# Performance work log

Measured on AMD Instinct MI355X. Metric: run time of the kernel, lower is better.

Reference implementation:

```python
import jax, jax.numpy as jnp
import numpy as np

B, S, HID = 2, 2048, 2048
NH, NKV, HD = 8, 1, 256
G = NH // NKV  # key-value groups
ROPE_BASE = 10000.0


def _rope_tables(seq_len, dim, base=ROPE_BASE):
    inv_freq = 1.0 / (base ** (jnp.arange(0, dim, 2, dtype=jnp.float32) / dim))
    t = jnp.arange(seq_len, dtype=jnp.float32)
    freqs = jnp.outer(t, inv_freq)            # [S, dim/2]
    emb = jnp.concatenate([freqs, freqs], -1)  # [S, dim]
    return jnp.cos(emb), jnp.sin(emb)


def _rotate_half(x):
    x1, x2 = jnp.split(x, 2, axis=-1)
    return jnp.concatenate([-x2, x1], axis=-1)


def setup_inputs() -> dict:
    key = jax.random.key(0)
    ks = jax.random.split(key, 6)
    hidden_states = jax.random.normal(ks[0], (B, S, HID), dtype=jnp.float32)
    # additive causal mask (0 on/below diagonal, -1e9 above)
    causal = jnp.triu(jnp.full((S, S), -1e9, dtype=jnp.float32), k=1)
    attention_mask = jnp.broadcast_to(causal[None, None], (B, 1, S, S))
    sc = 0.02
    Wq = jax.random.normal(ks[1], (HID, NH * HD), dtype=jnp.float32) * sc
    Wk = jax.random.normal(ks[2], (HID, NKV * HD), dtype=jnp.float32) * sc
    Wv = jax.random.normal(ks[3], (HID, NKV * HD), dtype=jnp.float32) * sc
    Wo = jax.random.normal(ks[4], (NH * HD, HID), dtype=jnp.float32) * sc
    return {"hidden_states": hidden_states, "attention_mask": attention_mask,
            "Wq": Wq, "Wk": Wk, "Wv": Wv, "Wo": Wo}


def reference(hidden_states, attention_mask, Wq, Wk, Wv, Wo):
    b, s, _ = hidden_states.shape
    q = (hidden_states @ Wq).reshape(b, s, NH, HD).transpose(0, 2, 1, 3)    # [B,NH,S,D]
    k = (hidden_states @ Wk).reshape(b, s, NKV, HD).transpose(0, 2, 1, 3)   # [B,NKV,S,D]
    v = (hidden_states @ Wv).reshape(b, s, NKV, HD).transpose(0, 2, 1, 3)
    cos, sin = _rope_tables(s, HD)
    cos, sin = cos[None, None], sin[None, None]
    q = q * cos + _rotate_half(q) * sin
    k = k * cos + _rotate_half(k) * sin
    # GQA: broadcast KV over groups instead of repeat_interleave (same math)
    qg = q.reshape(b, NKV, G, s, HD)
    scores = jnp.einsum('bkgqd,bkld->bkgql', qg, k) / np.sqrt(HD)  # [B,NKV,G,S,S]
    scores = scores + attention_mask[:, :, None]                    # mask broadcast over kv/groups
    probs = jax.nn.softmax(scores, axis=-1)
    out = jnp.einsum('bkgql,bkld->bkgqd', probs, v)                 # [B,NKV,G,S,D]
    out = out.reshape(b, NH, s, HD).transpose(0, 2, 1, 3).reshape(b, s, NH * HD)
    return out @ Wo
```

## Files before the change

kernel.cpp:

```cpp
#include <hip/hip_runtime.h>
#include <hip/hip_bf16.h>
#include <cstdint>
#include <cstddef>

#define DEVI __device__ __forceinline__

typedef __attribute__((ext_vector_type(8))) short short8;
typedef __attribute__((ext_vector_type(4))) float f32x4;

constexpr int BB = 2, SS = 2048, HID = 2048, NH = 8, HD = 256;
constexpr int M_TOT = BB * SS;
constexpr int RTOT = BB * NH * SS;

DEVI unsigned short f2bf(float f) {
  union { float f; unsigned int u; } v; v.f = f;
  unsigned int u = v.u;
  unsigned int r = (u + 0x7FFFu + ((u >> 16) & 1u)) >> 16;
  return (unsigned short)r;
}

DEVI float bf2f(unsigned short u) {
  union { unsigned int i; float f; } v; v.i = ((unsigned int)u) << 16;
  return v.f;
}

DEVI void gload_lds16(const void* g, void* l) {
  __builtin_amdgcn_global_load_lds(
      (const __attribute__((address_space(1))) unsigned int*)g,
      (__attribute__((address_space(3))) unsigned int*)l, 16, 0, 0);
}

__global__ void convert_f32_bf16(const float* __restrict__ in,
                                 unsigned short* __restrict__ out, int n8) {
  const int i = blockIdx.x * blockDim.x + threadIdx.x;
  if (i >= n8) return;
  const f32x4* p = (const f32x4*)in;
  f32x4 a = p[i * 2], b = p[i * 2 + 1];
  short8 o;
#pragma unroll
  for (int j = 0; j < 4; ++j) {
    o[j] = (short)f2bf(a[j]);
    o[j + 4] = (short)f2bf(b[j]);
  }
  ((short8*)out)[i] = o;
}

__global__ void transpose_w(const float* __restrict__ W,
                            unsigned short* __restrict__ Wt, int K, int N) {
  __shared__ float t[32][33];
  const int n0 = blockIdx.x * 32, k0 = blockIdx.y * 32;
  const int c = threadIdx.x & 31, r8 = threadIdx.x >> 5;
#pragma unroll
  for (int i = 0; i < 4; ++i) {
    const int r = r8 + i * 8;
    t[r][c] = W[(size_t)(k0 + r) * N + n0 + c];
  }
  __syncthreads();
#pragma unroll
  for (int i = 0; i < 4; ++i) {
    const int r = r8 + i * 8;
    Wt[(size_t)(n0 + r) * K + k0 + c] = f2bf(t[c][r]);
  }
}

__global__ void rope_table(float* __restrict__ ct, float* __restrict__ st) {
  const int i = blockIdx.x * blockDim.x + threadIdx.x;
  const int s = i >> 7, d = i & 127;
  const float inv = __expf(-(float)d * (9.210340371976184f / 128.0f));
  const float ang = (float)s * inv;
  float sn, cs;
  sincosf(ang, &sn, &cs);
  ct[i] = cs;
  st[i] = sn;
}

__global__ void rope_apply(unsigned short* __restrict__ X, const float* __restrict__ ct,
                           const float* __restrict__ st, int heads, int stride, int total) {
  const int i = blockIdx.x * blockDim.x + threadIdx.x;
  if (i >= total) return;
  const int d = i & 127;
  const int t = i >> 7;
  const int hh = t % heads;
  const int row = t / heads;
  const int s = row & (SS - 1);
  const size_t base = (size_t)row * stride + (size_t)hh * HD;
  const float q1 = bf2f(X[base + d]), q2 = bf2f(X[base + d + 128]);
  const float cs = ct[s * 128 + d], sn = st[s * 128 + d];
  X[base + d] = f2bf(q1 * cs - q2 * sn);
  X[base + d + 128] = f2bf(q2 * cs + q1 * sn);
}

template <int WMODE>
__global__ __launch_bounds__(256)
void gemm_bt(const unsigned short* __restrict__ A,
             const unsigned short* __restrict__ Bt,
             void* __restrict__ Cp, void* __restrict__ Cp2, void* __restrict__ Cp3,
             int N, int K) {
  __shared__ unsigned short As[128 * 32];
  __shared__ unsigned short Bs[128 * 32];
  const int tid = threadIdx.x;
  const int wid = tid >> 6, lane = tid & 63;
  const int wr = wid >> 1, wc = wid & 1;
  const int l15 = lane & 15, lg = lane >> 4;
  const int m0 = blockIdx.y * 128, n0 = blockIdx.x * 128;
  const int lrow = lane >> 2, lch = lane & 3;
  f32x4 acc[4][4];
#pragma unroll
  for (int i = 0; i < 4; ++i)
#pragma unroll
    for (int j = 0; j < 4; ++j) acc[i][j] = f32x4{0.f, 0.f, 0.f, 0.f};
  const unsigned short* Ab = A + (size_t)m0 * K;
  const unsigned short* Bb = Bt + (size_t)n0 * K;
  for (int k0 = 0; k0 < K; k0 += 32) {
    __syncthreads();
#pragma unroll
    for (int i = 0; i < 2; ++i) {
      const int rr = wid * 32 + i * 16;
      gload_lds16(Ab + (size_t)(rr + lrow) * K + k0 + lch * 8, &As[rr * 32]);
      gload_lds16(Bb + (size_t)(rr + lrow) * K + k0 + lch * 8, &Bs[rr * 32]);
    }
    asm volatile("s_waitcnt vmcnt(0)" ::: "memory");
    __syncthreads();
    short8 a[4], b[4];
#pragma unroll
    for (int m = 0; m < 4; ++m)
      a[m] = *(const short8*)&As[(wr * 64 + m * 16 + l15) * 32 + lg * 8];
#pragma unroll
    for (int n = 0; n < 4; ++n)
      b[n] = *(const short8*)&Bs[(wc * 64 + n * 16 + l15) * 32 + lg * 8];
#pragma unroll
    for (int m = 0; m < 4; ++m)
#pragma unroll
      for (int n = 0; n < 4; ++n)
        acc[m][n] = __builtin_amdgcn_mfma_f32_16x16x32_bf16(a[m], b[n], acc[m][n], 0, 0, 0);
  }
  const int row0 = m0 + wr * 64 + lg * 4;
  const int col0 = n0 + wc * 64 + l15;
#pragma unroll
  for (int m = 0; m < 4; ++m)
#pragma unroll
    for (int n = 0; n < 4; ++n)
#pragma unroll
      for (int r = 0; r < 4; ++r) {
        const int row = row0 + m * 16 + r;
        const int col = col0 + n * 16;
        const float v = acc[m][n][r];
        if (WMODE == 1) {
          ((float*)Cp)[(size_t)row * N + col] = v;
        } else {
          if (col < 2048)
            ((unsigned short*)Cp)[(size_t)row * 2048 + col] = f2bf(v);
          else if (col < 2304)
            ((unsigned short*)Cp2)[(size_t)row * 256 + (col - 2048)] = f2bf(v);
          else
            ((unsigned short*)Cp3)[((size_t)((row >> 11) * HD + (col - 2304))) * SS + (row & (SS - 1))] = f2bf(v);
        }
      }
}

__global__ __launch_bounds__(512)
void attn_split(const unsigned short* __restrict__ Q,
                const unsigned short* __restrict__ Kc,
                const unsigned short* __restrict__ Vt,
                float* __restrict__ Opart, float* __restrict__ Ml) {
  __shared__ unsigned short Ks[2][64 * 256];
  __shared__ unsigned short Vs[2][256 * 64];
  __shared__ unsigned short Ps[8][1024];
  const int tid = threadIdx.x;
  const int wid = tid >> 6, lane = tid & 63;
  const int l15 = lane & 15, lg = lane >> 4;
  const int pi = (int)blockIdx.x >> 1, s = (int)blockIdx.x & 1;
  const int h = blockIdx.y, b = blockIdx.z;
  const int qtA = pi, qtB = 15 - pi;

  short8 qf[8];
  f32x4 acc[16];
  float mrow[4], lrow[4];

  auto load_q = [&](int qt) {
    const int qrow = qt * 128 + wid * 16 + l15;
    const size_t qbase = ((size_t)(b * SS + qrow)) * (NH * HD) + (size_t)h * HD;
#pragma unroll
    for (int c = 0; c < 8; ++c)
      qf[c] = *(const short8*)&Q[qbase + c * 32 + lg * 8];
#pragma unroll
    for (int n = 0; n < 16; ++n) acc[n] = f32x4{0.f, 0.f, 0.f, 0.f};
#pragma unroll
    for (int r = 0; r < 4; ++r) { mrow[r] = -3e38f; lrow[r] = 0.f; }
  };

  auto write_part = [&](int qt) {
    const size_t rbase = ((size_t)(b * NH + h)) * SS + qt * 128 + wid * 16 + lg * 4;
#pragma unroll
    for (int n = 0; n < 16; ++n)
#pragma unroll
      for (int r = 0; r < 4; ++r)
        Opart[((size_t)s * RTOT + rbase + r) * 256 + n * 16 + l15] = acc[n][r];
    if (l15 == 0) {
#pragma unroll
      for (int r = 0; r < 4; ++r)
        ((float2*)Ml)[(size_t)s * RTOT + rbase + r] = float2{mrow[r], lrow[r]};
    }
  };

  auto stage = [&](int buf, int kv0) {
    unsigned short* KsB = &Ks[buf][0];
    unsigned short* VsB = &Vs[buf][0];
#pragma unroll
    for (int j = 0; j < 4; ++j) {
      {
        const int r0 = wid * 8 + j * 2;
        const int r = r0 + (lane >> 5), c = lane & 31;
        gload_lds16(Kc + ((size_t)(b * SS + kv0 + r)) * HD + ((c ^ (r & 7)) * 8),
                    &KsB[r0 * 256]);
      }
      {
        const int r0 = (wid * 4 + j) * 8;
        const int r = r0 + (lane >> 3), c = lane & 7;
        gload_lds16(Vt + ((size_t)(b * HD + r)) * SS + kv0 + ((c ^ (r & 7)) * 8),
                    &VsB[r0 * 64]);
      }
    }
  };

  auto compute = [&](int buf, int qt, int kv0) {
    const int wmax = qt * 128 + wid * 16 + 15;
    if (kv0 > wmax) return;
    const unsigned short* KsB = &Ks[buf][0];
    const unsigned short* VsB = &Vs[buf][0];
    f32x4 sf[4];
#pragma unroll
    for (int t = 0; t < 4; ++t) {
      f32x4 sv = {0.f, 0.f, 0.f, 0.f};
      const int kvr = t * 16 + l15;
      const char* krow = (const char*)KsB + kvr * 512;
      const int sw = (kvr & 7) << 4;
#pragma unroll
      for (int c = 0; c < 8; ++c) {
        short8 bf = *(const short8*)(krow + ((c * 64 + lg * 16) ^ sw));
        sv = __builtin_amdgcn_mfma_f32_16x16x32_bf16(qf[c], bf, sv, 0, 0, 0);
      }
      sf[t] = sv;
    }

    float pm[4] = {-3e38f, -3e38f, -3e38f, -3e38f};
    const int qr0 = qt * 128 + wid * 16 + lg * 4;
#pragma unroll
    for (int t = 0; t < 4; ++t) {
      const int kvc = kv0 + t * 16 + l15;
#pragma unroll
      for (int r = 0; r < 4; ++r) {
        float v = sf[t][r] * 0.0625f;
        v = (kvc > qr0 + r) ? -3e38f : v;
        sf[t][r] = v;
        pm[r] = fmaxf(pm[r], v);
      }
    }
    float scale[4];
    float growth = -3e38f;
#pragma unroll
    for (int r = 0; r < 4; ++r) {
      float v = pm[r];
      v = fmaxf(v, __shfl_xor(v, 1));
      v = fmaxf(v, __shfl_xor(v, 2));
      v = fmaxf(v, __shfl_xor(v, 4));
      v = fmaxf(v, __shfl_xor(v, 8));
      pm[r] = v;
      growth = fmaxf(growth, v - mrow[r]);
    }
    const bool norescale = __all(growth <= 0.f);
#pragma unroll
    for (int r = 0; r < 4; ++r) {
      const float mn = norescale ? mrow[r] : fmaxf(mrow[r], pm[r]);
      scale[r] = norescale ? 1.f : __expf(mrow[r] - mn);
      mrow[r] = mn;
      float sum = 0.f;
#pragma unroll
      for (int t = 0; t < 4; ++t) {
        const float p = __expf(sf[t][r] - mn);
        sf[t][r] = p;
        sum += p;
      }
      sum += __shfl_xor(sum, 1);
      sum += __shfl_xor(sum, 2);
      sum += __shfl_xor(sum, 4);
      sum += __shfl_xor(sum, 8);
      lrow[r] = lrow[r] * scale[r] + sum;
    }
    if (!norescale) {
#pragma unroll
      for (int n = 0; n < 16; ++n)
#pragma unroll
        for (int r = 0; r < 4; ++r) acc[n][r] *= scale[r];
    }

    char* pw = (char*)&Ps[wid][0];
#pragma unroll
    for (int t = 0; t < 4; ++t)
#pragma unroll
      for (int r = 0; r < 4; ++r) {
        const int q = lg * 4 + r;
        *(unsigned short*)(pw + q * 128 + (((t * 16 + l15) * 2) ^ ((q & 7) << 4))) =
            f2bf(sf[t][r]);
      }
    asm volatile("s_waitcnt lgkmcnt(0)" ::: "memory");
    short8 pf[2];
    {
      const char* pr = pw + l15 * 128;
      const int sw = (l15 & 7) << 4;
      pf[0] = *(const short8*)(pr + ((lg * 16) ^ sw));
      pf[1] = *(const short8*)(pr + ((64 + lg * 16) ^ sw));
    }
#pragma unroll
    for (int n = 0; n < 16; ++n) {
      const int dr = n * 16 + l15;
      const char* vrow = (const char*)VsB + dr * 128;
      const int sw = (dr & 7) << 4;
      short8 v0 = *(const short8*)(vrow + ((lg * 16) ^ sw));
      short8 v1 = *(const short8*)(vrow + ((64 + lg * 16) ^ sw));
      acc[n] = __builtin_amdgcn_mfma_f32_16x16x32_bf16(pf[0], v0, acc[n], 0, 0, 0);
      acc[n] = __builtin_amdgcn_mfma_f32_16x16x32_bf16(pf[1], v1, acc[n], 0, 0, 0);
    }
  };

  auto kv_of = [&](int i) {
    const int j = (i <= qtA) ? i : (i - qtA - 1);
    return (s + 2 * j) * 64;
  };

  load_q(qtA);
  stage(0, kv_of(0));
  asm volatile("s_waitcnt vmcnt(0)" ::: "memory");
  __syncthreads();
  int buf = 0;
  for (int i = 0; i < 17; ++i) {
    if (i + 1 < 17) stage(buf ^ 1, kv_of(i + 1));
    if (i == qtA + 1) {
      write_part(qtA);
      load_q(qtB);
    }
    const int qt = (i <= qtA) ? qtA : qtB;
    compute(buf, qt, kv_of(i));
    asm volatile("s_waitcnt vmcnt(0)" ::: "memory");
    __syncthreads();
    buf ^= 1;
  }
  write_part(qtB);
}

__global__ void merge_splits(const float* __restrict__ Opart,
                             const float* __restrict__ Ml,
                             unsigned short* __restrict__ AO) {
  const int gid = blockIdx.x * 256 + threadIdx.x;
  const int ridx = gid >> 5;
  const int d0 = (gid & 31) * 8;
  const float2 ab0 = ((const float2*)Ml)[ridx];
  const float2 ab1 = ((const float2*)Ml)[RTOT + ridx];
  const float M = fmaxf(ab0.x, ab1.x);
  const float w0 = __expf(ab0.x - M), w1 = __expf(ab1.x - M);
  const float inv = 1.f / (w0 * ab0.y + w1 * ab1.y);
  const float4* o0 = (const float4*)&Opart[(size_t)ridx * 256 + d0];
  const float4* o1 = (const float4*)&Opart[((size_t)RTOT + ridx) * 256 + d0];
  float4 a0 = o0[0], a1 = o0[1], b0 = o1[0], b1 = o1[1];
  const int b = ridx >> 14, rem = ridx & 16383;
  const int h = rem >> 11, srow = rem & 2047;
  short8 o;
#pragma unroll
  for (int j = 0; j < 4; ++j) {
    o[j] = (short)f2bf((w0 * a0[j] + w1 * b0[j]) * inv);
    o[j + 4] = (short)f2bf((w0 * a1[j] + w1 * b1[j]) * inv);
  }
  *(short8*)(AO + ((size_t)(b * SS + srow)) * (NH * HD) + (size_t)h * HD + d0) = o;
}

__global__ __launch_bounds__(256)
void attn_fb(const unsigned short* __restrict__ Q,
             const unsigned short* __restrict__ Kc,
             const unsigned short* __restrict__ Vt,
             unsigned short* __restrict__ AO) {
  __shared__ unsigned short Ks[2][64 * 256];
  __shared__ unsigned short Vs[2][256 * 64];
  __shared__ unsigned short Ps[4][1024];
  const int tid = threadIdx.x;
  const int wid = tid >> 6, lane = tid & 63;
  const int l15 = lane & 15, lg = lane >> 4;
  const int qtA = (int)blockIdx.x;
  const int qtB = 31 - qtA;
  const int h = blockIdx.y, b = blockIdx.z;

  short8 qf[8];
  f32x4 acc[16];
  float mrow[4], lrow[4];

  auto load_q = [&](int qt) {
    const int qrow = qt * 64 + wid * 16 + l15;
    const size_t qbase = ((size_t)(b * SS + qrow)) * (NH * HD) + (size_t)h * HD;
#pragma unroll
    for (int c = 0; c < 8; ++c)
      qf[c] = *(const short8*)&Q[qbase + c * 32 + lg * 8];
#pragma unroll
    for (int n = 0; n < 16; ++n) acc[n] = f32x4{0.f, 0.f, 0.f, 0.f};
#pragma unroll
    for (int r = 0; r < 4; ++r) { mrow[r] = -3e38f; lrow[r] = 0.f; }
  };

  auto write_o = [&](int qt) {
    float invl[4];
#pragma unroll
    for (int r = 0; r < 4; ++r) invl[r] = 1.f / lrow[r];
    const int orow0 = b * SS + qt * 64 + wid * 16 + lg * 4;
#pragma unroll
    for (int n = 0; n < 16; ++n)
#pragma unroll
      for (int r = 0; r < 4; ++r)
        AO[(size_t)(orow0 + r) * (NH * HD) + (size_t)h * HD + n * 16 + l15] =
            f2bf(acc[n][r] * invl[r]);
  };

  auto stage = [&](int buf, int kv0) {
    unsigned short* KsB = &Ks[buf][0];
    unsigned short* VsB = &Vs[buf][0];
#pragma unroll
    for (int j = 0; j < 8; ++j) {
      {
        const int r0 = wid * 16 + j * 2;
        const int r = r0 + (lane >> 5), c = lane & 31;
        gload_lds16(Kc + ((size_t)(b * SS + kv0 + r)) * HD + ((c ^ (r & 7)) * 8),
                    &KsB[r0 * 256]);
      }
      {
        const int r0 = (wid * 8 + j) * 8;
        const int r = r0 + (lane >> 3), c = lane & 7;
        gload_lds16(Vt + ((size_t)(b * HD + r)) * SS + kv0 + ((c ^ (r & 7)) * 8),
                    &VsB[r0 * 64]);
      }
    }
  };

  auto compute = [&](int buf, int qt, int kv0) {
    const int wmax = qt * 64 + wid * 16 + 15;
    if (kv0 > wmax) return;
    const unsigned short* KsB = &Ks[buf][0];
    const unsigned short* VsB = &Vs[buf][0];
    f32x4 sf[4];
#pragma unroll
    for (int t = 0; t < 4; ++t) {
      f32x4 sv = {0.f, 0.f, 0.f, 0.f};
      const int kvr = t * 16 + l15;
      const char* krow = (const char*)KsB + kvr * 512;
      const int sw = (kvr & 7) << 4;
#pragma unroll
      for (int c = 0; c < 8; ++c) {
        short8 bf = *(const short8*)(krow + ((c * 64 + lg * 16) ^ sw));
        sv = __builtin_amdgcn_mfma_f32_16x16x32_bf16(qf[c], bf, sv, 0, 0, 0);
      }
      sf[t] = sv;
    }
    float pm[4] = {-3e38f, -3e38f, -3e38f, -3e38f};
    const int qr0 = qt * 64 + wid * 16 + lg * 4;
#pragma unroll
    for (int t = 0; t < 4; ++t) {
      const int kvc = kv0 + t * 16 + l15;
#pragma unroll
      for (int r = 0; r < 4; ++r) {
        float v = sf[t][r] * 0.0625f;
        v = (kvc > qr0 + r) ? -3e38f : v;
        sf[t][r] = v;
        pm[r] = fmaxf(pm[r], v);
      }
    }
    float scale[4];
    float growth = -3e38f;
#pragma unroll
    for (int r = 0; r < 4; ++r) {
      float v = pm[r];
      v = fmaxf(v, __shfl_xor(v, 1));
      v = fmaxf(v, __shfl_xor(v, 2));
      v = fmaxf(v, __shfl_xor(v, 4));
      v = fmaxf(v, __shfl_xor(v, 8));
      pm[r] = v;
      growth = fmaxf(growth, v - mrow[r]);
    }
    const bool norescale = __all(growth <= 0.f);
#pragma unroll
    for (int r = 0; r < 4; ++r) {
      const float mn = norescale ? mrow[r] : fmaxf(mrow[r], pm[r]);
      scale[r] = norescale ? 1.f : __expf(mrow[r] - mn);
      mrow[r] = mn;
      float sum = 0.f;
#pragma unroll
      for (int t = 0; t < 4; ++t) {
        const float p = __expf(sf[t][r] - mn);
        sf[t][r] = p;
        sum += p;
      }
      sum += __shfl_xor(sum, 1);
      sum += __shfl_xor(sum, 2);
      sum += __shfl_xor(sum, 4);
      sum += __shfl_xor(sum, 8);
      lrow[r] = lrow[r] * scale[r] + sum;
    }
    if (!norescale) {
#pragma unroll
      for (int n = 0; n < 16; ++n)
#pragma unroll
        for (int r = 0; r < 4; ++r) acc[n][r] *= scale[r];
    }
    char* pw = (char*)&Ps[wid][0];
#pragma unroll
    for (int t = 0; t < 4; ++t)
#pragma unroll
      for (int r = 0; r < 4; ++r) {
        const int q = lg * 4 + r;
        *(unsigned short*)(pw + q * 128 + (((t * 16 + l15) * 2) ^ ((q & 7) << 4))) =
            f2bf(sf[t][r]);
      }
    asm volatile("s_waitcnt lgkmcnt(0)" ::: "memory");
    short8 pf[2];
    {
      const char* pr = pw + l15 * 128;
      const int sw = (l15 & 7) << 4;
      pf[0] = *(const short8*)(pr + ((lg * 16) ^ sw));
      pf[1] = *(const short8*)(pr + ((64 + lg * 16) ^ sw));
    }
#pragma unroll
    for (int n = 0; n < 16; ++n) {
      const int dr = n * 16 + l15;
      const char* vrow = (const char*)VsB + dr * 128;
      const int sw = (dr & 7) << 4;
      short8 v0 = *(const short8*)(vrow + ((lg * 16) ^ sw));
      short8 v1 = *(const short8*)(vrow + ((64 + lg * 16) ^ sw));
      acc[n] = __builtin_amdgcn_mfma_f32_16x16x32_bf16(pf[0], v0, acc[n], 0, 0, 0);
      acc[n] = __builtin_amdgcn_mfma_f32_16x16x32_bf16(pf[1], v1, acc[n], 0, 0, 0);
    }
  };

  const int nA = qtA + 1;
  load_q(qtA);
  int curq = qtA;
  stage(0, 0);
  asm volatile("s_waitcnt vmcnt(0)" ::: "memory");
  __syncthreads();
  int buf = 0;
  for (int i = 0; i < 33; ++i) {
    const int t0 = (i >= nA) ? (i - nA) : i;
    if (i + 1 < 33) {
      const int t0n = (i + 1 >= nA) ? (i + 1 - nA) : (i + 1);
      stage(buf ^ 1, t0n * 64);
    }
    if (i >= nA && curq == qtA) {
      write_o(qtA);
      load_q(qtB);
      curq = qtB;
    }
    compute(buf, curq, t0 * 64);
    asm volatile("s_waitcnt vmcnt(0)" ::: "memory");
    __syncthreads();
    buf ^= 1;
  }
  write_o(qtB);
}

extern "C" void kernel_launch(void* const* d_in, const int* in_sizes, int n_in,
                              void* d_out, int out_size, void* d_ws, size_t ws_size,
                              hipStream_t stream) {
  (void)in_sizes; (void)n_in; (void)out_size;
  const float* hs = (const float*)d_in[0];
  const float* Wq = (const float*)d_in[2];
  const float* Wk = (const float*)d_in[3];
  const float* Wv = (const float*)d_in[4];
  const float* Wo = (const float*)d_in[5];

  char* ws = (char*)d_ws;
  size_t off = 0;
  auto alloc = [&](size_t bytes) -> void* {
    void* p = ws + off;
    off += (bytes + 255) & ~(size_t)255;
    return p;
  };
  unsigned short* Xb  = (unsigned short*)alloc((size_t)M_TOT * HID * 2);
  unsigned short* WqT = (unsigned short*)alloc((size_t)2048 * 2048 * 2);
  unsigned short* WkT = (unsigned short*)alloc((size_t)256 * 2048 * 2);
  unsigned short* WvT = (unsigned short*)alloc((size_t)256 * 2048 * 2);
  unsigned short* WoT = (unsigned short*)alloc((size_t)2048 * 2048 * 2);
  unsigned short* Qb  = (unsigned short*)alloc((size_t)M_TOT * 2048 * 2);
  unsigned short* Kb  = (unsigned short*)alloc((size_t)M_TOT * 256 * 2);
  unsigned short* Vtw = (unsigned short*)alloc((size_t)M_TOT * 256 * 2);
  float* ct = (float*)alloc((size_t)SS * 128 * 4);
  float* st = (float*)alloc((size_t)SS * 128 * 4);
  float* Opart = (float*)alloc((size_t)2 * RTOT * 256 * 4);
  float* Mlb   = (float*)alloc((size_t)2 * RTOT * 2 * 4);
  const bool use_split = ws_size >= off;
  unsigned short* AO = Xb;

  convert_f32_bf16<<<M_TOT * HID / 8 / 256, 256, 0, stream>>>(hs, Xb, M_TOT * HID / 8);
  transpose_w<<<dim3(2048 / 32, 2048 / 32), 256, 0, stream>>>(Wq, WqT, 2048, 2048);
  transpose_w<<<dim3(256 / 32, 2048 / 32), 256, 0, stream>>>(Wk, WkT, 2048, 256);
  transpose_w<<<dim3(256 / 32, 2048 / 32), 256, 0, stream>>>(Wv, WvT, 2048, 256);
  transpose_w<<<dim3(2048 / 32, 2048 / 32), 256, 0, stream>>>(Wo, WoT, 2048, 2048);
  rope_table<<<SS * 128 / 256, 256, 0, stream>>>(ct, st);

  gemm_bt<4><<<dim3(2560 / 128, M_TOT / 128), 256, 0, stream>>>(Xb, WqT, Qb, Kb, Vtw, 2560, 2048);

  rope_apply<<<(M_TOT * NH * 128) / 256, 256, 0, stream>>>(Qb, ct, st, NH, 2048, M_TOT * NH * 128);
  rope_apply<<<(M_TOT * 128) / 256, 256, 0, stream>>>(Kb, ct, st, 1, 256, M_TOT * 128);

  if (use_split) {
    attn_split<<<dim3(16, NH, BB), 512, 0, stream>>>(Qb, Kb, Vtw, Opart, Mlb);
    merge_splits<<<RTOT * 32 / 256, 256, 0, stream>>>(Opart, Mlb, AO);
  } else {
    attn_fb<<<dim3(16, NH, BB), 256, 0, stream>>>(Qb, Kb, Vtw, AO);
  }

  gemm_bt<1><<<dim3(2048 / 128, M_TOT / 128), 256, 0, stream>>>(AO, WoT, d_out, nullptr, nullptr, 2048, 2048);
}
```

Measured before the change: 252.8 us.

## Widen GEMM K-tile with swizzled LDS, bf16 split partials, exp2 softmax, setprio

```diff
diff --git a/kernel.cpp b/kernel.cpp
--- a/kernel.cpp
+++ b/kernel.cpp
@@ -11,6 +11,7 @@
 constexpr int BB = 2, SS = 2048, HID = 2048, NH = 8, HD = 256;
 constexpr int M_TOT = BB * SS;
 constexpr int RTOT = BB * NH * SS;
+constexpr float SM_SCALE_LOG2 = 0.09016844005556021f;
 
 DEVI unsigned short f2bf(float f) {
   union { float f; unsigned int u; } v; v.f = f;
@@ -96,14 +97,14 @@
              const unsigned short* __restrict__ Bt,
              void* __restrict__ Cp, void* __restrict__ Cp2, void* __restrict__ Cp3,
              int N, int K) {
-  __shared__ unsigned short As[128 * 32];
-  __shared__ unsigned short Bs[128 * 32];
+  __shared__ unsigned short As[128 * 64];
+  __shared__ unsigned short Bs[128 * 64];
   const int tid = threadIdx.x;
   const int wid = tid >> 6, lane = tid & 63;
   const int wr = wid >> 1, wc = wid & 1;
   const int l15 = lane & 15, lg = lane >> 4;
   const int m0 = blockIdx.y * 128, n0 = blockIdx.x * 128;
-  const int lrow = lane >> 2, lch = lane & 3;
+  const int lrow = lane >> 3, lch = lane & 7;
   f32x4 acc[4][4];
 #pragma unroll
   for (int i = 0; i < 4; ++i)
@@ -111,28 +112,36 @@
     for (int j = 0; j < 4; ++j) acc[i][j] = f32x4{0.f, 0.f, 0.f, 0.f};
   const unsigned short* Ab = A + (size_t)m0 * K;
   const unsigned short* Bb = Bt + (size_t)n0 * K;
-  for (int k0 = 0; k0 < K; k0 += 32) {
+  for (int k0 = 0; k0 < K; k0 += 64) {
     __syncthreads();
 #pragma unroll
-    for (int i = 0; i < 2; ++i) {
-      const int rr = wid * 32 + i * 16;
-      gload_lds16(Ab + (size_t)(rr + lrow) * K + k0 + lch * 8, &As[rr * 32]);
-      gload_lds16(Bb + (size_t)(rr + lrow) * K + k0 + lch * 8, &Bs[rr * 32]);
+    for (int i = 0; i < 4; ++i) {
+      const int r0 = wid * 32 + i * 8;
+      const int r = r0 + lrow;
+      gload_lds16(Ab + (size_t)r * K + k0 + ((lch ^ (r & 7)) * 8), &As[r0 * 64]);
+      gload_lds16(Bb + (size_t)r * K + k0 + ((lch ^ (r & 7)) * 8), &Bs[r0 * 64]);
     }
     asm volatile("s_waitcnt vmcnt(0)" ::: "memory");
     __syncthreads();
-    short8 a[4], b[4];
-#pragma unroll
-    for (int m = 0; m < 4; ++m)
-      a[m] = *(const short8*)&As[(wr * 64 + m * 16 + l15) * 32 + lg * 8];
-#pragma unroll
-    for (int n = 0; n < 4; ++n)
-      b[n] = *(const short8*)&Bs[(wc * 64 + n * 16 + l15) * 32 + lg * 8];
-#pragma unroll
-    for (int m = 0; m < 4; ++m)
-#pragma unroll
-      for (int n = 0; n < 4; ++n)
-        acc[m][n] = __builtin_amdgcn_mfma_f32_16x16x32_bf16(a[m], b[n], acc[m][n], 0, 0, 0);
+#pragma unroll
+    for (int kk = 0; kk < 2; ++kk) {
+      short8 a[4], b[4];
+#pragma unroll
+      for (int m = 0; m < 4; ++m) {
+        const int row = wr * 64 + m * 16 + l15;
+        a[m] = *(const short8*)&As[row * 64 + (((kk * 4 + lg) ^ (row & 7)) * 8)];
+      }
+#pragma unroll
+      for (int n = 0; n < 4; ++n) {
+        const int row = wc * 64 + n * 16 + l15;
+        b[n] = *(const short8*)&Bs[row * 64 + (((kk * 4 + lg) ^ (row & 7)) * 8)];
+      }
+#pragma unroll
+      for (int m = 0; m < 4; ++m)
+#pragma unroll
+        for (int n = 0; n < 4; ++n)
+          acc[m][n] = __builtin_amdgcn_mfma_f32_16x16x32_bf16(a[m], b[n], acc[m][n], 0, 0, 0);
+    }
   }
   const int row0 = m0 + wr * 64 + lg * 4;
   const int col0 = n0 + wc * 64 + l15;
@@ -162,7 +171,7 @@
 void attn_split(const unsigned short* __restrict__ Q,
                 const unsigned short* __restrict__ Kc,
                 const unsigned short* __restrict__ Vt,
-                float* __restrict__ Opart, float* __restrict__ Ml) {
+                unsigned short* __restrict__ Opart, float* __restrict__ Ml) {
   __shared__ unsigned short Ks[2][64 * 256];
   __shared__ unsigned short Vs[2][256 * 64];
   __shared__ unsigned short Ps[8][1024];
@@ -195,7 +204,7 @@
     for (int n = 0; n < 16; ++n)
 #pragma unroll
       for (int r = 0; r < 4; ++r)
-        Opart[((size_t)s * RTOT + rbase + r) * 256 + n * 16 + l15] = acc[n][r];
+        Opart[((size_t)s * RTOT + rbase + r) * 256 + n * 16 + l15] = f2bf(acc[n][r]);
     if (l15 == 0) {
 #pragma unroll
       for (int r = 0; r < 4; ++r)
@@ -229,6 +238,7 @@
     const unsigned short* KsB = &Ks[buf][0];
     const unsigned short* VsB = &Vs[buf][0];
     f32x4 sf[4];
+    __builtin_amdgcn_s_setprio(1);
 #pragma unroll
     for (int t = 0; t < 4; ++t) {
       f32x4 sv = {0.f, 0.f, 0.f, 0.f};
@@ -242,6 +252,7 @@
       }
       sf[t] = sv;
     }
+    __builtin_amdgcn_s_setprio(0);
 
     float pm[4] = {-3e38f, -3e38f, -3e38f, -3e38f};
     const int qr0 = qt * 128 + wid * 16 + lg * 4;
@@ -250,7 +261,7 @@
       const int kvc = kv0 + t * 16 + l15;
 #pragma unroll
       for (int r = 0; r < 4; ++r) {
-        float v = sf[t][r] * 0.0625f;
+        float v = sf[t][r] * SM_SCALE_LOG2;
         v = (kvc > qr0 + r) ? -3e38f : v;
         sf[t][r] = v;
         pm[r] = fmaxf(pm[r], v);
@@ -272,12 +283,12 @@
 #pragma unroll
     for (int r = 0; r < 4; ++r) {
       const float mn = norescale ? mrow[r] : fmaxf(mrow[r], pm[r]);
-      scale[r] = norescale ? 1.f : __expf(mrow[r] - mn);
+      scale[r] = norescale ? 1.f : exp2f(mrow[r] - mn);
       mrow[r] = mn;
       float sum = 0.f;
 #pragma unroll
       for (int t = 0; t < 4; ++t) {
-        const float p = __expf(sf[t][r] - mn);
+        const float p = exp2f(sf[t][r] - mn);
         sf[t][r] = p;
         sum += p;
       }
@@ -311,6 +322,7 @@
       pf[0] = *(const short8*)(pr + ((lg * 16) ^ sw));
       pf[1] = *(const short8*)(pr + ((64 + lg * 16) ^ sw));
     }
+    __builtin_amdgcn_s_setprio(1);
 #pragma unroll
     for (int n = 0; n < 16; ++n) {
       const int dr = n * 16 + l15;
@@ -321,6 +333,7 @@
       acc[n] = __builtin_amdgcn_mfma_f32_16x16x32_bf16(pf[0], v0, acc[n], 0, 0, 0);
       acc[n] = __builtin_amdgcn_mfma_f32_16x16x32_bf16(pf[1], v1, acc[n], 0, 0, 0);
     }
+    __builtin_amdgcn_s_setprio(0);
   };
 
   auto kv_of = [&](int i) {
@@ -348,7 +361,7 @@
   write_part(qtB);
 }
 
-__global__ void merge_splits(const float* __restrict__ Opart,
+__global__ void merge_splits(const unsigned short* __restrict__ Opart,
                              const float* __restrict__ Ml,
                              unsigned short* __restrict__ AO) {
   const int gid = blockIdx.x * 256 + threadIdx.x;
@@ -357,19 +370,17 @@
   const float2 ab0 = ((const float2*)Ml)[ridx];
   const float2 ab1 = ((const float2*)Ml)[RTOT + ridx];
   const float M = fmaxf(ab0.x, ab1.x);
-  const float w0 = __expf(ab0.x - M), w1 = __expf(ab1.x - M);
+  const float w0 = exp2f(ab0.x - M), w1 = exp2f(ab1.x - M);
   const float inv = 1.f / (w0 * ab0.y + w1 * ab1.y);
-  const float4* o0 = (const float4*)&Opart[(size_t)ridx * 256 + d0];
-  const float4* o1 = (const float4*)&Opart[((size_t)RTOT + ridx) * 256 + d0];
-  float4 a0 = o0[0], a1 = o0[1], b0 = o1[0], b1 = o1[1];
+  const short8 p0 = *(const short8*)&Opart[(size_t)ridx * 256 + d0];
+  const short8 p1 = *(const short8*)&Opart[((size_t)RTOT + ridx) * 256 + d0];
   const int b = ridx >> 14, rem = ridx & 16383;
   const int h = rem >> 11, srow = rem & 2047;
   short8 o;
 #pragma unroll
-  for (int j = 0; j < 4; ++j) {
-    o[j] = (short)f2bf((w0 * a0[j] + w1 * b0[j]) * inv);
-    o[j + 4] = (short)f2bf((w0 * a1[j] + w1 * b1[j]) * inv);
-  }
+  for (int j = 0; j < 8; ++j)
+    o[j] = (short)f2bf((w0 * bf2f((unsigned short)p0[j]) +
+                        w1 * bf2f((unsigned short)p1[j])) * inv);
   *(short8*)(AO + ((size_t)(b * SS + srow)) * (NH * HD) + (size_t)h * HD + d0) = o;
 }
 
@@ -588,8 +599,8 @@
   unsigned short* Vtw = (unsigned short*)alloc((size_t)M_TOT * 256 * 2);
   float* ct = (float*)alloc((size_t)SS * 128 * 4);
   float* st = (float*)alloc((size_t)SS * 128 * 4);
-  float* Opart = (float*)alloc((size_t)2 * RTOT * 256 * 4);
-  float* Mlb   = (float*)alloc((size_t)2 * RTOT * 2 * 4);
+  unsigned short* Opart = (unsigned short*)alloc((size_t)2 * RTOT * 256 * 2);
+  float* Mlb = (float*)alloc((size_t)2 * RTOT * 2 * 4);
   const bool use_split = ws_size >= off;
   unsigned short* AO = Xb;
 
```

Result: faster. 237.1 us (-6.2%).
